# Kernel tuning notes

Measured on AMD Instinct MI355X. Metric: run time of the kernel, lower is better.

Reference implementation:

```python
import jax, jax.numpy as jnp
import numpy as np

NUM_HEADS = 4
D_MODEL = 256
HEAD_DIM = D_MODEL // NUM_HEADS  # 64
B, N = 8, 2048


def _proj(x, W, b):
    # Conv1d with kernel_size=1 == pointwise linear over channel dim
    # x: [B, C_in, N], W: [C_out, C_in], b: [C_out]
    return jnp.einsum('oi,bin->bon', W, x) + b[None, :, None]


def setup_inputs() -> dict:
    key = jax.random.key(0)
    ks = jax.random.split(key, 11)
    s = 1.0 / np.sqrt(D_MODEL)
    return {
        'query': jax.random.normal(ks[0], (B, D_MODEL, N), jnp.float32),
        'key':   jax.random.normal(ks[1], (B, D_MODEL, N), jnp.float32),
        'value': jax.random.normal(ks[2], (B, D_MODEL, N), jnp.float32),
        'Wq': jax.random.normal(ks[3], (D_MODEL, D_MODEL), jnp.float32) * s,
        'bq': jax.random.normal(ks[4], (D_MODEL,), jnp.float32) * 0.01,
        'Wk': jax.random.normal(ks[5], (D_MODEL, D_MODEL), jnp.float32) * s,
        'bk': jax.random.normal(ks[6], (D_MODEL,), jnp.float32) * 0.01,
        'Wv': jax.random.normal(ks[7], (D_MODEL, D_MODEL), jnp.float32) * s,
        'bv': jax.random.normal(ks[8], (D_MODEL,), jnp.float32) * 0.01,
        'Wm': jax.random.normal(ks[9], (D_MODEL, D_MODEL), jnp.float32) * s,
        'bm': jax.random.normal(ks[10], (D_MODEL,), jnp.float32) * 0.01,
    }


def reference(query, key, value, Wq, bq, Wk, bk, Wv, bv, Wm, bm):
    b = query.shape[0]
    # project then split channels into (head_dim, num_heads): [B, d, h, N]
    q = _proj(query, Wq, bq).reshape(b, HEAD_DIM, NUM_HEADS, -1)
    k = _proj(key,   Wk, bk).reshape(b, HEAD_DIM, NUM_HEADS, -1)
    v = _proj(value, Wv, bv).reshape(b, HEAD_DIM, NUM_HEADS, -1)
    scale = 1.0 / jnp.sqrt(jnp.asarray(HEAD_DIM, q.dtype))
    scores = jnp.einsum('bdhn,bdhm->bhnm', q, k) * scale  # [B,H,N,N]
    prob = jax.nn.softmax(scores, axis=-1)
    x = jnp.einsum('bhnm,bdhm->bdhn', prob, v)  # [B,d,H,N]
    x = x.reshape(b, HEAD_DIM * NUM_HEADS, -1)  # [B, d_model, N]
    return _proj(x, Wm, bm)
```

## Files before the change

kernel.cpp:

```cpp
#include <hip/hip_runtime.h>
#include <math.h>


constexpr int BATCH  = 8;
constexpr int DMODEL = 256;
constexpr int SEQ    = 2048;
constexpr int HDIM   = 64;
constexpr int TN     = 128;
constexpr int TM     = 64;
constexpr int NJT    = SEQ / TM;

typedef _Float16 half2_t __attribute__((ext_vector_type(2)));
typedef _Float16 half4_t __attribute__((ext_vector_type(4)));
typedef _Float16 half8_t __attribute__((ext_vector_type(8)));
typedef float    float4_t __attribute__((ext_vector_type(4)));

static __device__ __forceinline__ void ld16_lds(const void* g, void* l) {
    __builtin_amdgcn_global_load_lds(
        (const __attribute__((address_space(1))) unsigned*)g,
        (__attribute__((address_space(3))) unsigned*)l, 16, 0, 0);
}

static __device__ __forceinline__ half8_t cvt8(const float4 w0, const float4 w1) {
    half8_t a;
    a[0] = (_Float16)w0.x; a[1] = (_Float16)w0.y;
    a[2] = (_Float16)w0.z; a[3] = (_Float16)w0.w;
    a[4] = (_Float16)w1.x; a[5] = (_Float16)w1.y;
    a[6] = (_Float16)w1.z; a[7] = (_Float16)w1.w;
    return a;
}

__global__ __launch_bounds__(256, 3)
void gemm_qkv(const float* __restrict__ Wq, const float* __restrict__ Wk,
              const float* __restrict__ Wv,
              const float* __restrict__ bq, const float* __restrict__ bk,
              const float* __restrict__ bv,
              const float* __restrict__ Xq, const float* __restrict__ Xk,
              const float* __restrict__ Xv, _Float16* __restrict__ qT,
              _Float16* __restrict__ kT, _Float16* __restrict__ vT)
{
    const int n0 = blockIdx.x * 64;
    const int proj = blockIdx.y >> 3, b = blockIdx.y & 7;
    const float* W    = proj == 0 ? Wq : proj == 1 ? Wk : Wv;
    const float* bias = proj == 0 ? bq : proj == 1 ? bk : bv;
    const float* X    = (proj == 0 ? Xq : proj == 1 ? Xk : Xv)
                        + (size_t)b * DMODEL * SEQ;
    const float qs = (proj == 0) ? 0.18033688011112042f : 1.0f;

    __shared__ __align__(16) char lds[50432];
    float*    T  = (float*)lds;
    _Float16* Xs = (_Float16*)(lds + 16640);
    _Float16* Tw = (_Float16*)lds;

    const int tid = threadIdx.x, tn = tid & 15, tc = tid >> 4;

    #pragma unroll
    for (int cc = 0; cc < 4; ++cc) {
        __syncthreads();
        #pragma unroll
        for (int i = 0; i < 4; ++i) {
            const int c = tc + 16 * i;
            const float4 v = *(const float4*)&X[(size_t)(cc * 64 + c) * SEQ + n0 + tn * 4];
            T[c * 65 + tn * 4 + 0] = v.x; T[c * 65 + tn * 4 + 1] = v.y;
            T[c * 65 + tn * 4 + 2] = v.z; T[c * 65 + tn * 4 + 3] = v.w;
        }
        __syncthreads();
        #pragma unroll
        for (int i = 0; i < 4; ++i) {
            const int n = tc + 16 * i;
            half4_t h4;
            #pragma unroll
            for (int j = 0; j < 4; ++j) h4[j] = (_Float16)T[(tn * 4 + j) * 65 + n];
            *(half4_t*)&Xs[n * 264 + cc * 64 + tn * 4] = h4;
        }
    }
    __syncthreads();

    const int w = tid >> 6, lane = tid & 63;
    const int lm = lane & 15, g = lane >> 4, g8 = g * 8;
    const int cw0 = w * 64;

    float4_t acc[4][4];
    #pragma unroll
    for (int mt = 0; mt < 4; ++mt)
        #pragma unroll
        for (int nt = 0; nt < 4; ++nt) acc[mt][nt] = (float4_t){0.f, 0.f, 0.f, 0.f};

    #pragma unroll
    for (int k0 = 0; k0 < DMODEL; k0 += 64) {
        half8_t a[4][2], bb[4][2];
        #pragma unroll
        for (int mt = 0; mt < 4; ++mt)
            #pragma unroll
            for (int kd = 0; kd < 2; ++kd) {
                const float* wp = &W[(size_t)(cw0 + mt * 16 + lm) * DMODEL
                                     + k0 + kd * 32 + g8];
                a[mt][kd] = cvt8(*(const float4*)wp, *(const float4*)(wp + 4));
            }
        #pragma unroll
        for (int nt = 0; nt < 4; ++nt)
            #pragma unroll
            for (int kd = 0; kd < 2; ++kd)
                bb[nt][kd] = *(const half8_t*)&Xs[(nt * 16 + lm) * 264
                                                  + k0 + kd * 32 + g8];
        #pragma unroll
        for (int kd = 0; kd < 2; ++kd)
            #pragma unroll
            for (int mt = 0; mt < 4; ++mt)
                #pragma unroll
                for (int nt = 0; nt < 4; ++nt)
                    acc[mt][nt] = __builtin_amdgcn_mfma_f32_16x16x32_f16(
                        a[mt][kd], bb[nt][kd], acc[mt][nt], 0, 0, 0);
    }
    __syncthreads();

    #pragma unroll
    for (int mt = 0; mt < 4; ++mt) {
        const float4 b4 = *(const float4*)&bias[cw0 + mt * 16 + g * 4];
        const float bb4[4] = {b4.x, b4.y, b4.z, b4.w};
        #pragma unroll
        for (int nt = 0; nt < 4; ++nt) {
            half4_t pk;
            #pragma unroll
            for (int r = 0; r < 4; ++r)
                pk[r] = (_Float16)((acc[mt][nt][r] + bb4[r]) * qs);
            *(half4_t*)&Tw[((w * 64 + nt * 16 + lm)) * 68 + mt * 16 + g * 4] = pk;
        }
    }

    if (proj < 2) {
        _Float16* dst = (proj == 0 ? qT : kT);
        const int h2 = lane >> 4, lml = lane & 15;
        #pragma unroll
        for (int it = 0; it < 4; ++it) {
            const int nl = it * 16 + lml;
            const int hs = (nl & 3) | (((nl >> 3) & 1) << 2);
            #pragma unroll
            for (int dc = 0; dc < 2; ++dc) {
                half8_t ch;
                #pragma unroll
                for (int e = 0; e < 8; ++e)
                    ch[e] = Tw[(w * 64 + nl) * 68 + 4 * (dc * 8 + e) + h2];
                const int chunk = (w * 2 + dc) ^ hs;
                *(half8_t*)&dst[((size_t)(b * 4 + h2) * SEQ + n0 + nl) * HDIM
                                + chunk * 8] = ch;
            }
        }
    } else {
        const int hh = lane & 3, dl = (lane >> 2) & 15;
        const int d = w * 16 + dl;
        const size_t rowbase =
            (((size_t)(b * 4 + hh) * NJT + (n0 >> 6)) * HDIM + d) * (size_t)TM;
        #pragma unroll
        for (int jc = 0; jc < 8; ++jc) {
            half8_t ch;
            #pragma unroll
            for (int e = 0; e < 8; ++e)
                ch[e] = Tw[(w * 64 + jc * 8 + e) * 68 + 4 * dl + hh];
            *(half8_t*)&vT[rowbase + ((jc ^ (dl & 7)) << 3)] = ch;
        }
    }
}

__global__ __launch_bounds__(256, 4)
void attn_f16(const _Float16* __restrict__ qT, const _Float16* __restrict__ kT,
              const _Float16* __restrict__ vT, _Float16* __restrict__ xa,
              _Float16* __restrict__ xb, float* __restrict__ rs)
{
    const int lid = blockIdx.x;
    const int work = (lid & 7) * 128 + (lid >> 3);
    const int bh = work >> 5, b = bh >> 2, h = bh & 3;
    const int jh = (work >> 4) & 1;
    const int ib = work & 15;
    const int tid = threadIdx.x, wid = tid >> 6, lane = tid & 63;
    const int lm = lane & 15, g = lane >> 4;
    const int i0 = ib * TN + wid * 32;

    __shared__ _Float16 Kb[2][TM * HDIM];
    __shared__ _Float16 Vb[2][TM * HDIM];

    const int hq = (lm & 3) | (((lm >> 3) & 1) << 2);
    const int hk = (lm & 3) | (((lm >> 2) & 1) << 2);
    const int rbase = 8 * (lm >> 2) + (lm & 3);

    half8_t bq[2][2];
    const _Float16* qbase = qT + (size_t)bh * SEQ * HDIM;
    #pragma unroll
    for (int rt = 0; rt < 2; ++rt)
        #pragma unroll
        for (int kd = 0; kd < 2; ++kd) {
            const int row = i0 + rt * 16 + lm;
            bq[rt][kd] = *(const half8_t*)(qbase + (size_t)row * HDIM
                                           + (((kd * 4 + g) ^ hq) << 3));
        }

    const char* kt = (const char*)(kT + ((size_t)bh * SEQ + jh * (SEQ / 2)) * HDIM);
    const char* vt = (const char*)(vT + ((size_t)bh * NJT + jh * 16) * TM * HDIM);

    float4_t o[2][4];
    float rsum[2][2] = {{0.f, 0.f}, {0.f, 0.f}};
    #pragma unroll
    for (int rt = 0; rt < 2; ++rt)
        #pragma unroll
        for (int dt = 0; dt < 4; ++dt) o[rt][dt] = (float4_t){0.f, 0.f, 0.f, 0.f};

    #define STAGE(jt, bu)                                                     \
        {                                                                     \
            const char* kg = kt + (size_t)(jt) * 8192;                        \
            const char* vg = vt + (size_t)(jt) * 8192;                        \
            _Pragma("unroll")                                                 \
            for (int p = 0; p < 2; ++p) {                                     \
                const int c = wid + p * 4;                                    \
                ld16_lds(kg + c * 1024 + lane * 16, (char*)&Kb[bu][0] + c * 1024); \
                ld16_lds(vg + c * 1024 + lane * 16, (char*)&Vb[bu][0] + c * 1024); \
            }                                                                 \
        }

    STAGE(0, 0);
    __syncthreads();

    for (int jt = 0; jt < 16; ++jt) {
        const int cur = jt & 1;
        if (jt + 1 < 16) STAGE(jt + 1, cur ^ 1);

        float4_t s[2][2][2];
        #pragma unroll
        for (int jb = 0; jb < 2; ++jb)
            #pragma unroll
            for (int u = 0; u < 2; ++u)
                #pragma unroll
                for (int rt = 0; rt < 2; ++rt)
                    s[jb][u][rt] = (float4_t){0.f, 0.f, 0.f, 0.f};
        #pragma unroll
        for (int kd = 0; kd < 2; ++kd)
            #pragma unroll
            for (int jb = 0; jb < 2; ++jb)
                #pragma unroll
                for (int u = 0; u < 2; ++u) {
                    const int jrow = jb * 32 + rbase + 4 * u;
                    const half8_t fk = *(const half8_t*)
                        &Kb[cur][jrow * HDIM + (((kd * 4 + g) ^ hk) << 3)];
                    #pragma unroll
                    for (int rt = 0; rt < 2; ++rt)
                        s[jb][u][rt] = __builtin_amdgcn_mfma_f32_16x16x32_f16(
                            fk, bq[rt][kd], s[jb][u][rt], 0, 0, 0);
                }

        half8_t ap[2][2];
        #pragma unroll
        for (int jb = 0; jb < 2; ++jb)
            #pragma unroll
            for (int rt = 0; rt < 2; ++rt) {
                half8_t p;
                #pragma unroll
                for (int r = 0; r < 4; ++r) {
                    const float e0 = __builtin_amdgcn_exp2f(s[jb][0][rt][r]);
                    const float e1 = __builtin_amdgcn_exp2f(s[jb][1][rt][r]);
                    rsum[jb][rt] += e0;
                    rsum[jb][rt] += e1;
                    p[r]     = (_Float16)e0;
                    p[r + 4] = (_Float16)e1;
                }
                ap[jb][rt] = p;
            }

        #pragma unroll
        for (int jb = 0; jb < 2; ++jb)
            #pragma unroll
            for (int dt = 0; dt < 4; ++dt) {
                const int d = dt * 16 + lm;
                const half8_t fv = *(const half8_t*)
                    &Vb[cur][d * TM + (((jb * 4 + g) ^ (lm & 7)) << 3)];
                #pragma unroll
                for (int rt = 0; rt < 2; ++rt)
                    o[rt][dt] = __builtin_amdgcn_mfma_f32_16x16x32_f16(
                        ap[jb][rt], fv, o[rt][dt], 0, 0, 0);
            }
        __syncthreads();
    }

    _Float16* xp = jh ? xb : xa;
    #pragma unroll
    for (int rt = 0; rt < 2; ++rt)
        #pragma unroll
        for (int dt = 0; dt < 4; ++dt) {
            const int c = 4 * (dt * 16 + lm) + h;
            #pragma unroll
            for (int r = 0; r < 4; ++r) {
                const int n = i0 + rt * 16 + 4 * g + r;
                xp[((size_t)b * SEQ + n) * DMODEL + c] = (_Float16)o[rt][dt][r];
            }
        }
    #pragma unroll
    for (int rt = 0; rt < 2; ++rt) {
        float v = rsum[0][rt] + rsum[1][rt];
        v += __shfl_xor(v, 16);
        v += __shfl_xor(v, 32);
        if (g == 0)
            rs[((size_t)jh * 32 + bh) * SEQ + i0 + rt * 16 + lm] = v;
    }
    #undef STAGE
}

__global__ __launch_bounds__(256)
void gemm_final(const float* __restrict__ Wm, const float* __restrict__ bias,
                const _Float16* __restrict__ xa, const _Float16* __restrict__ xb,
                const float* __restrict__ rs, float* __restrict__ out)
{
    const int n0 = blockIdx.x * 64, m0 = blockIdx.y * 128;
    const int b = blockIdx.z;
    const int tid = threadIdx.x, w = tid >> 6, lane = tid & 63;
    const int lm = lane & 15, g = lane >> 4, g8 = g * 8;
    const int cw0 = m0 + w * 32;

    __shared__ _Float16 Xc[64 * DMODEL];

    {
        const int c8 = tid & 31, nb = tid >> 5;
        const _Float16* Pa = xa + ((size_t)b * SEQ + n0) * DMODEL;
        const _Float16* Pb = xb + ((size_t)b * SEQ + n0) * DMODEL;
        #pragma unroll
        for (int j = 0; j < 8; ++j) {
            const int n = nb * 8 + j;
            const size_t off = (size_t)n * DMODEL + c8 * 8;
            const half8_t va = *(const half8_t*)&Pa[off];
            const half8_t vb = *(const half8_t*)&Pb[off];
            const half8_t sv = va + vb;
            *(half8_t*)&Xc[n * DMODEL + ((c8 ^ (n & 7)) << 3)] = sv;
        }
    }

    half8_t pm[4];
    #pragma unroll
    for (int nt = 0; nt < 4; ++nt) {
        const int n = n0 + nt * 16 + lm;
        #pragma unroll
        for (int hh = 0; hh < 4; ++hh) {
            const float l = rs[(size_t)(b * 4 + hh) * SEQ + n]
                          + rs[(size_t)(32 + b * 4 + hh) * SEQ + n];
            const _Float16 iv = (_Float16)(1.0f / l);
            pm[nt][hh] = iv; pm[nt][hh + 4] = iv;
        }
    }
    __syncthreads();

    float4_t acc[2][4];
    #pragma unroll
    for (int mt = 0; mt < 2; ++mt)
        #pragma unroll
        for (int nt = 0; nt < 4; ++nt) acc[mt][nt] = (float4_t){0.f, 0.f, 0.f, 0.f};

    #pragma unroll
    for (int k0 = 0; k0 < DMODEL; k0 += 64) {
        half8_t a[2][2], bb[4][2];
        #pragma unroll
        for (int mt = 0; mt < 2; ++mt)
            #pragma unroll
            for (int kd = 0; kd < 2; ++kd) {
                const float* wp = &Wm[(size_t)(cw0 + mt * 16 + lm) * DMODEL
                                      + k0 + kd * 32 + g8];
                a[mt][kd] = cvt8(*(const float4*)wp, *(const float4*)(wp + 4));
            }
        #pragma unroll
        for (int nt = 0; nt < 4; ++nt)
            #pragma unroll
            for (int kd = 0; kd < 2; ++kd) {
                const int n = nt * 16 + lm;
                const int c8 = (k0 >> 3) + kd * 4 + g;
                const half8_t sv = *(const half8_t*)
                    &Xc[n * DMODEL + ((c8 ^ (n & 7)) << 3)];
                bb[nt][kd] = sv * pm[nt];
            }
        #pragma unroll
        for (int kd = 0; kd < 2; ++kd)
            #pragma unroll
            for (int mt = 0; mt < 2; ++mt)
                #pragma unroll
                for (int nt = 0; nt < 4; ++nt)
                    acc[mt][nt] = __builtin_amdgcn_mfma_f32_16x16x32_f16(
                        a[mt][kd], bb[nt][kd], acc[mt][nt], 0, 0, 0);
    }

    #pragma unroll
    for (int mt = 0; mt < 2; ++mt)
        #pragma unroll
        for (int r = 0; r < 4; ++r) {
            const int co = cw0 + mt * 16 + g * 4 + r;
            const float bv_ = bias[co];
            #pragma unroll
            for (int nt = 0; nt < 4; ++nt)
                out[((size_t)b * DMODEL + co) * SEQ + n0 + nt * 16 + lm] =
                    acc[mt][nt][r] + bv_;
        }
}

extern "C" void kernel_launch(void* const* d_in, const int* in_sizes, int n_in,
                              void* d_out, int out_size, void* d_ws, size_t ws_size,
                              hipStream_t stream) {
    const float* query = (const float*)d_in[0];
    const float* key_  = (const float*)d_in[1];
    const float* value = (const float*)d_in[2];
    const float* Wq = (const float*)d_in[3];  const float* bq = (const float*)d_in[4];
    const float* Wk = (const float*)d_in[5];  const float* bk = (const float*)d_in[6];
    const float* Wv = (const float*)d_in[7];  const float* bv = (const float*)d_in[8];
    const float* Wm = (const float*)d_in[9];  const float* bm = (const float*)d_in[10];
    float* out = (float*)d_out;

    const size_t bufElems = (size_t)BATCH * DMODEL * SEQ;
    _Float16* qT = (_Float16*)d_ws;
    _Float16* kT = qT + bufElems;
    _Float16* vT = kT + bufElems;
    _Float16* xa = vT + bufElems;
    _Float16* xb = xa + bufElems;
    float*    rsb = (float*)(xb + bufElems);

    gemm_qkv<<<dim3(SEQ / 64, 3 * BATCH), 256, 0, stream>>>(
        Wq, Wk, Wv, bq, bk, bv, query, key_, value, qT, kT, vT);
    attn_f16<<<dim3(1024), 256, 0, stream>>>(qT, kT, vT, xa, xb, rsb);
    gemm_final<<<dim3(SEQ / 64, 2, BATCH), 256, 0, stream>>>(
        Wm, bm, xa, xb, rsb, out);
}
```

Before: 185.7 us.

## Make attention output head-contiguous and prepermute Wm to fp16 in QKV kernel

Extra blocks in the QKV projection kernel convert Wm to fp16 with its columns permuted into head-major order. The attention kernel can then write its output contiguously per head (h*64+d) instead of interleaving with stride 4. The final GEMM loads the fp16 weights directly, dropping the fp32 load and conversion, and applies a per-head scalar normalizer. The QKV epilogue also remaps lanes so each warp handles one head, with an extra barrier added. The cost is one more grid row of blocks plus the added synchronization.

```diff
diff --git a/kernel.cpp b/kernel.cpp
--- a/kernel.cpp
+++ b/kernel.cpp
@@ -32,13 +32,27 @@
 
 __global__ __launch_bounds__(256, 3)
 void gemm_qkv(const float* __restrict__ Wq, const float* __restrict__ Wk,
-              const float* __restrict__ Wv,
+              const float* __restrict__ Wv, const float* __restrict__ Wm,
               const float* __restrict__ bq, const float* __restrict__ bk,
               const float* __restrict__ bv,
               const float* __restrict__ Xq, const float* __restrict__ Xk,
               const float* __restrict__ Xv, _Float16* __restrict__ qT,
-              _Float16* __restrict__ kT, _Float16* __restrict__ vT)
+              _Float16* __restrict__ kT, _Float16* __restrict__ vT,
+              _Float16* __restrict__ wfp)
 {
+    if (blockIdx.y == 24) {
+        const int r = blockIdx.x * 8 + (threadIdx.x >> 5);
+        const int c32 = threadIdx.x & 31;
+        half8_t o8;
+        #pragma unroll
+        for (int e = 0; e < 8; ++e) {
+            const int hd = c32 * 8 + e;
+            o8[e] = (_Float16)Wm[r * DMODEL + 4 * (hd & 63) + (hd >> 6)];
+        }
+        *(half8_t*)&wfp[(size_t)r * DMODEL + c32 * 8] = o8;
+        return;
+    }
+
     const int n0 = blockIdx.x * 64;
     const int proj = blockIdx.y >> 3, b = blockIdx.y & 7;
     const float* W    = proj == 0 ? Wq : proj == 1 ? Wk : Wv;
@@ -127,37 +141,41 @@
             *(half4_t*)&Tw[((w * 64 + nt * 16 + lm)) * 68 + mt * 16 + g * 4] = pk;
         }
     }
+    __syncthreads();
 
     if (proj < 2) {
         _Float16* dst = (proj == 0 ? qT : kT);
-        const int h2 = lane >> 4, lml = lane & 15;
-        #pragma unroll
-        for (int it = 0; it < 4; ++it) {
-            const int nl = it * 16 + lml;
+        const int h = w;
+        const int dcg = lane & 7, nlb = lane >> 3;
+        #pragma unroll
+        for (int it = 0; it < 8; ++it) {
+            const int nl = it * 8 + nlb;
             const int hs = (nl & 3) | (((nl >> 3) & 1) << 2);
-            #pragma unroll
-            for (int dc = 0; dc < 2; ++dc) {
-                half8_t ch;
-                #pragma unroll
-                for (int e = 0; e < 8; ++e)
-                    ch[e] = Tw[(w * 64 + nl) * 68 + 4 * (dc * 8 + e) + h2];
-                const int chunk = (w * 2 + dc) ^ hs;
-                *(half8_t*)&dst[((size_t)(b * 4 + h2) * SEQ + n0 + nl) * HDIM
-                                + chunk * 8] = ch;
-            }
+            half8_t ch;
+            #pragma unroll
+            for (int e = 0; e < 8; ++e) {
+                ch[e] = Tw[((dcg >> 1) * 64 + nl) * 68
+                           + 4 * ((dcg & 1) * 8 + e) + h];
+            }
+            const int chunk = dcg ^ hs;
+            *(half8_t*)&dst[((size_t)(b * 4 + h) * SEQ + n0 + nl) * HDIM
+                            + chunk * 8] = ch;
         }
     } else {
-        const int hh = lane & 3, dl = (lane >> 2) & 15;
-        const int d = w * 16 + dl;
-        const size_t rowbase =
-            (((size_t)(b * 4 + hh) * NJT + (n0 >> 6)) * HDIM + d) * (size_t)TM;
-        #pragma unroll
-        for (int jc = 0; jc < 8; ++jc) {
+        const int h = w;
+        const int jc = lane & 7, db = lane >> 3;
+        const size_t tilebase =
+            (((size_t)(b * 4 + h) * NJT + (n0 >> 6)) * HDIM) * (size_t)TM;
+        #pragma unroll
+        for (int it = 0; it < 8; ++it) {
+            const int d = it * 8 + db;
             half8_t ch;
             #pragma unroll
-            for (int e = 0; e < 8; ++e)
-                ch[e] = Tw[(w * 64 + jc * 8 + e) * 68 + 4 * dl + hh];
-            *(half8_t*)&vT[rowbase + ((jc ^ (dl & 7)) << 3)] = ch;
+            for (int e = 0; e < 8; ++e) {
+                ch[e] = Tw[((d >> 4) * 64 + jc * 8 + e) * 68
+                           + 4 * (d & 15) + h];
+            }
+            *(half8_t*)&vT[tilebase + (size_t)d * TM + ((jc ^ (d & 7)) << 3)] = ch;
         }
     }
 }
@@ -284,11 +302,12 @@
     for (int rt = 0; rt < 2; ++rt)
         #pragma unroll
         for (int dt = 0; dt < 4; ++dt) {
-            const int c = 4 * (dt * 16 + lm) + h;
+            const int d = dt * 16 + lm;
             #pragma unroll
             for (int r = 0; r < 4; ++r) {
                 const int n = i0 + rt * 16 + 4 * g + r;
-                xp[((size_t)b * SEQ + n) * DMODEL + c] = (_Float16)o[rt][dt][r];
+                xp[((size_t)b * SEQ + n) * DMODEL + h * HDIM + d] =
+                    (_Float16)o[rt][dt][r];
             }
         }
     #pragma unroll
@@ -303,7 +322,7 @@
 }
 
 __global__ __launch_bounds__(256)
-void gemm_final(const float* __restrict__ Wm, const float* __restrict__ bias,
+void gemm_final(const _Float16* __restrict__ wfp, const float* __restrict__ bias,
                 const _Float16* __restrict__ xa, const _Float16* __restrict__ xb,
                 const float* __restrict__ rs, float* __restrict__ out)
 {
@@ -330,7 +349,7 @@
         }
     }
 
-    half8_t pm[4];
+    _Float16 pmh[4][4];
     #pragma unroll
     for (int nt = 0; nt < 4; ++nt) {
         const int n = n0 + nt * 16 + lm;
@@ -338,8 +357,7 @@
         for (int hh = 0; hh < 4; ++hh) {
             const float l = rs[(size_t)(b * 4 + hh) * SEQ + n]
                           + rs[(size_t)(32 + b * 4 + hh) * SEQ + n];
-            const _Float16 iv = (_Float16)(1.0f / l);
-            pm[nt][hh] = iv; pm[nt][hh + 4] = iv;
+            pmh[nt][hh] = (_Float16)(1.0f / l);
         }
     }
     __syncthreads();
@@ -356,11 +374,9 @@
         #pragma unroll
         for (int mt = 0; mt < 2; ++mt)
             #pragma unroll
-            for (int kd = 0; kd < 2; ++kd) {
-                const float* wp = &Wm[(size_t)(cw0 + mt * 16 + lm) * DMODEL
-                                      + k0 + kd * 32 + g8];
-                a[mt][kd] = cvt8(*(const float4*)wp, *(const float4*)(wp + 4));
-            }
+            for (int kd = 0; kd < 2; ++kd)
+                a[mt][kd] = *(const half8_t*)&wfp[(size_t)(cw0 + mt * 16 + lm) * DMODEL
+                                                  + k0 + kd * 32 + g8];
         #pragma unroll
         for (int nt = 0; nt < 4; ++nt)
             #pragma unroll
@@ -369,7 +385,8 @@
                 const int c8 = (k0 >> 3) + kd * 4 + g;
                 const half8_t sv = *(const half8_t*)
                     &Xc[n * DMODEL + ((c8 ^ (n & 7)) << 3)];
-                bb[nt][kd] = sv * pm[nt];
+                const int hh = (k0 + kd * 32 + g8) >> 6;
+                bb[nt][kd] = sv * pmh[nt][hh];
             }
         #pragma unroll
         for (int kd = 0; kd < 2; ++kd)
@@ -413,10 +430,11 @@
     _Float16* xa = vT + bufElems;
     _Float16* xb = xa + bufElems;
     float*    rsb = (float*)(xb + bufElems);
-
-    gemm_qkv<<<dim3(SEQ / 64, 3 * BATCH), 256, 0, stream>>>(
-        Wq, Wk, Wv, bq, bk, bv, query, key_, value, qT, kT, vT);
+    _Float16* wfp = (_Float16*)(rsb + 2 * 32 * SEQ);
+
+    gemm_qkv<<<dim3(SEQ / 64, 25), 256, 0, stream>>>(
+        Wq, Wk, Wv, Wm, bq, bk, bv, query, key_, value, qT, kT, vT, wfp);
     attn_f16<<<dim3(1024), 256, 0, stream>>>(qT, kT, vT, xa, xb, rsb);
     gemm_final<<<dim3(SEQ / 64, 2, BATCH), 256, 0, stream>>>(
-        Wm, bm, xa, xb, rsb, out);
-}
+        wfp, bm, xa, xb, rsb, out);
+}
```

New measurement: 175.3 us. 1.06x faster.
